# Kernel optimization log

Measured on AMD Instinct MI355X. Metric: run time of the kernel, lower is better.

The kernel has to match this reference:

```python
import jax, jax.numpy as jnp
import numpy as np

B, S, D, H = 2, 2048, 1024, 16
HD = D // H

def setup_inputs() -> dict:
    key = jax.random.key(0)
    ks = jax.random.split(key, 9)
    s = 1.0 / np.sqrt(D)
    inp = {"x": jax.random.normal(ks[0], (B, S, D), dtype=jnp.float32)}
    for i, name in enumerate(["q", "k", "v", "o"]):
        inp[f"W_{name}"] = jax.random.uniform(ks[1 + 2 * i], (D, D), dtype=jnp.float32, minval=-s, maxval=s)
        inp[f"b_{name}"] = jax.random.uniform(ks[2 + 2 * i], (D,), dtype=jnp.float32, minval=-s, maxval=s)
    return inp


def reference(x, W_q, b_q, W_k, b_k, W_v, b_v, W_o, b_o):
    # x: [B, S, D]
    def split_heads(t):
        return t.reshape(B, S, H, HD).transpose(0, 2, 1, 3)  # [B, H, S, HD]

    Q = split_heads(x @ W_q + b_q)
    K = split_heads(x @ W_k + b_k)
    V = split_heads(x @ W_v + b_v)

    scale = 1.0 / np.sqrt(HD).astype(np.float32)
    scores = jnp.einsum("bhqd,bhkd->bhqk", Q, K) * scale  # [B, H, S, S]
    weights = jax.nn.softmax(scores, axis=-1)
    attn = jnp.einsum("bhqk,bhkd->bhqd", weights, V)  # [B, H, S, HD]
    attn = attn.transpose(0, 2, 1, 3).reshape(B, S, D)
    return attn @ W_o + b_o
```

## Files before the change

kernel.cpp:

```cpp
#include <hip/hip_runtime.h>
#include <hip/hip_bf16.h>

#define BB 2
#define SS 2048
#define DD 1024
#define HH 16
#define HD 64

typedef __attribute__((ext_vector_type(8))) short bf16x8;
typedef __attribute__((ext_vector_type(4))) float f32x4;

__device__ __forceinline__ unsigned short f2bf(float f) {
  unsigned int u = __float_as_uint(f);
  return (unsigned short)((u + 0x7FFFu + ((u >> 16) & 1u)) >> 16);
}

__device__ __forceinline__ float fast_exp2(float x) {
#if __has_builtin(__builtin_amdgcn_exp2f)
  return __builtin_amdgcn_exp2f(x);
#else
  return __expf(x * 0.6931471805599453f);
#endif
}

__device__ __forceinline__ void async_copy16(const unsigned short* gp, unsigned short* lp) {
  __builtin_amdgcn_global_load_lds(
      (const __attribute__((address_space(1))) unsigned int*)gp,
      (__attribute__((address_space(3))) unsigned int*)lp, 16, 0, 0);
}

__device__ __forceinline__ void pl32_swap(unsigned& a, unsigned& b) {
#if __has_builtin(__builtin_amdgcn_permlane32_swap)
  auto r = __builtin_amdgcn_permlane32_swap(a, b, false, false);
  a = r[0];
  b = r[1];
#else
  asm volatile("v_permlane32_swap_b32 %0, %1" : "+v"(a), "+v"(b));
#endif
}
__device__ __forceinline__ void pl16_swap(unsigned& a, unsigned& b) {
#if __has_builtin(__builtin_amdgcn_permlane16_swap)
  auto r = __builtin_amdgcn_permlane16_swap(a, b, false, false);
  a = r[0];
  b = r[1];
#else
  asm volatile("v_permlane16_swap_b32 %0, %1" : "+v"(a), "+v"(b));
#endif
}

__global__ __launch_bounds__(256) void prep_kernel(
    const float* __restrict__ x, unsigned short* __restrict__ xb,
    const float* __restrict__ W0, unsigned short* __restrict__ T0,
    const float* __restrict__ W1, unsigned short* __restrict__ T1,
    const float* __restrict__ W2, unsigned short* __restrict__ T2,
    const float* __restrict__ W3, unsigned short* __restrict__ T3) {
  const int blk = blockIdx.x;
  const int t = threadIdx.x;
  if (blk < 4096) {
    int i = blk * 1024 + t * 4;
    float4 v = *(const float4*)(x + i);
    ushort4 u;
    u.x = f2bf(v.x); u.y = f2bf(v.y); u.z = f2bf(v.z); u.w = f2bf(v.w);
    *(ushort4*)(xb + i) = u;
    return;
  }
  const int j = blk - 4096;
  const int jw = j >> 10;
  const int tb = j & 1023;
  const float* W = jw == 0 ? W0 : (jw == 1 ? W1 : (jw == 2 ? W2 : W3));
  unsigned short* T = jw == 0 ? T0 : (jw == 1 ? T1 : (jw == 2 ? T2 : T3));
  __shared__ float tile[32][33];
  int k0 = (tb & 31) * 32, n0 = (tb >> 5) * 32;
  int c = t & 31, r0 = t >> 5;
#pragma unroll
  for (int i = 0; i < 4; ++i) {
    int r = r0 + i * 8;
    tile[r][c] = W[(size_t)(k0 + r) * DD + n0 + c];
  }
  __syncthreads();
#pragma unroll
  for (int i = 0; i < 4; ++i) {
    int r = r0 + i * 8;
    T[(size_t)(n0 + r) * DD + k0 + c] = f2bf(tile[c][r]);
  }
}

template <int STORE>
__device__ __forceinline__ void gemm_core(
    const unsigned short* __restrict__ A, const unsigned short* __restrict__ BT,
    const float* __restrict__ bias, void* __restrict__ outp, float scale,
    int bm, int bn) {
  const int t = threadIdx.x;
  const int w = t >> 6;
  const int l = t & 63;
  const int wm = (w >> 1) * 64;
  const int wn = (w & 1) * 64;

  __shared__ __align__(16) unsigned short As[128 * 32];
  __shared__ __align__(16) unsigned short Bs[128 * 32];

  f32x4 acc[4][4];
#pragma unroll
  for (int i = 0; i < 4; ++i)
#pragma unroll
    for (int j = 0; j < 4; ++j) acc[i][j] = (f32x4)0.f;

  const int fr = l & 15;
  const int kg = (l >> 4) * 8;

  for (int k0 = 0; k0 < DD; k0 += 32) {
    __syncthreads();
#pragma unroll
    for (int c = 0; c < 2; ++c) {
      int e = (w * 2 + c) * 512 + l * 8;
      int row = e >> 5, kk = e & 31;
      async_copy16(A + (size_t)(bm + row) * DD + k0 + kk, As + (w * 2 + c) * 512);
      async_copy16(BT + (size_t)(bn + row) * DD + k0 + kk, Bs + (w * 2 + c) * 512);
    }
    __syncthreads();

    bf16x8 af[4], bfr[4];
#pragma unroll
    for (int i = 0; i < 4; ++i)
      af[i] = *(const bf16x8*)(As + (wm + i * 16 + fr) * 32 + kg);
#pragma unroll
    for (int j = 0; j < 4; ++j)
      bfr[j] = *(const bf16x8*)(Bs + (wn + j * 16 + fr) * 32 + kg);
#pragma unroll
    for (int i = 0; i < 4; ++i)
#pragma unroll
      for (int j = 0; j < 4; ++j)
        acc[i][j] = __builtin_amdgcn_mfma_f32_16x16x32_bf16(af[i], bfr[j], acc[i][j], 0, 0, 0);
  }

  const int col_l = l & 15;
  const int row_l = (l >> 4) * 4;

#pragma unroll
  for (int i = 0; i < 4; ++i) {
    int m_base = bm + wm + i * 16 + row_l;
#pragma unroll
    for (int j = 0; j < 4; ++j) {
      int n = bn + wn + j * 16 + col_l;
      float bv = bias[n];
      float* out = (float*)outp;
#pragma unroll
      for (int r = 0; r < 4; ++r)
        out[(size_t)(m_base + r) * DD + n] = acc[i][j][r] + bv;
    }
  }
}

__global__ __launch_bounds__(256) void out_gemm_mfma(
    const unsigned short* __restrict__ A, const unsigned short* __restrict__ WoT,
    const float* __restrict__ bo, float* __restrict__ out) {
  const int i = blockIdx.x;
  const int xcd = i & 7;
  const int slot = i >> 3;
  const int bm = (xcd + 8 * (slot >> 3)) * 128;
  const int bn = (slot & 7) * 128;
  gemm_core<0>(A, WoT, bo, (void*)out, 1.0f, bm, bn);
}

__global__ __launch_bounds__(256, 3) void qkv_gemm_tri(
    const unsigned short* __restrict__ A,
    const unsigned short* __restrict__ WqT, const unsigned short* __restrict__ WkT,
    const unsigned short* __restrict__ WvT,
    const float* __restrict__ bq, const float* __restrict__ bk,
    const float* __restrict__ bv,
    unsigned short* __restrict__ Qo, unsigned short* __restrict__ Ko,
    unsigned short* __restrict__ VTo) {
  const int i = blockIdx.x;
  const int xcd = i & 7;
  const int slot = i >> 3;
  const int bm = (xcd + 8 * (slot / 24)) * 128;
  const int c = slot % 24;
  const int which = c >> 3;
  const int bn = (c & 7) * 128;
  const unsigned short* BT = which == 0 ? WqT : (which == 1 ? WkT : WvT);
  const float* bias = which == 0 ? bq : (which == 1 ? bk : bv);

  const int t = threadIdx.x;
  const int w = t >> 6;
  const int l = t & 63;
  const int wm = (w >> 1) * 64;
  const int wn = (w & 1) * 64;
  const int fr = l & 15;
  const int kgB = (l >> 4) * 16;

  __shared__ __align__(16) unsigned short lds[2][3][4096];

  f32x4 acc[4][4];
#pragma unroll
  for (int ii = 0; ii < 4; ++ii)
#pragma unroll
    for (int j = 0; j < 4; ++j) acc[ii][j] = (f32x4)0.f;

  int aoff[4], boff[4];
#pragma unroll
  for (int ii = 0; ii < 4; ++ii) {
    aoff[ii] = (wm + ii * 16 + fr) * 64 + kgB;
    boff[ii] = (wn + ii * 16 + fr) * 64 + kgB;
  }

  const int cc0 = w * 128 + l;
  const int cc1 = cc0 + 64;
  const int row0 = cc0 >> 2, kk0 = (cc0 & 3) * 8;
  const int row1 = cc1 >> 2, kk1 = (cc1 & 3) * 8;
  const unsigned short* a0 = A + (size_t)(bm + row0) * DD + kk0;
  const unsigned short* a1 = A + (size_t)(bm + row1) * DD + kk1;
  const unsigned short* b0 = BT + (size_t)(bn + row0) * DD + kk0;
  const unsigned short* b1 = BT + (size_t)(bn + row1) * DD + kk1;

  auto stage_tile = [&](int T) {
    if (T >= 32) return;
    const int buf = T % 3;
    const int k0 = T * 32;
    async_copy16(a0 + k0, &lds[0][buf][w * 1024]);
    async_copy16(a1 + k0, &lds[0][buf][w * 1024 + 512]);
    async_copy16(b0 + k0, &lds[1][buf][w * 1024]);
    async_copy16(b1 + k0, &lds[1][buf][w * 1024 + 512]);
  };

  auto phase = [&](int T, int vm) {
    const int buf = T % 3;
    const char* Ab = (const char*)&lds[0][buf][0];
    const char* Bb = (const char*)&lds[1][buf][0];
    bf16x8 af[4], bfr[4];
#pragma unroll
    for (int ii = 0; ii < 4; ++ii) af[ii] = *(const bf16x8*)(Ab + aoff[ii]);
#pragma unroll
    for (int j = 0; j < 4; ++j) bfr[j] = *(const bf16x8*)(Bb + boff[j]);
    stage_tile(T + 2);
    asm volatile("s_barrier" ::: "memory");
    __builtin_amdgcn_s_setprio(1);
#pragma unroll
    for (int ii = 0; ii < 4; ++ii)
#pragma unroll
      for (int j = 0; j < 4; ++j)
        acc[ii][j] = __builtin_amdgcn_mfma_f32_16x16x32_bf16(af[ii], bfr[j], acc[ii][j], 0, 0, 0);
    __builtin_amdgcn_s_setprio(0);
    if (vm == 1) asm volatile("s_waitcnt vmcnt(4)" ::: "memory");
    if (vm == 2) asm volatile("s_waitcnt vmcnt(0)" ::: "memory");
    asm volatile("s_barrier" ::: "memory");
  };

  stage_tile(0);
  stage_tile(1);
  asm volatile("s_waitcnt vmcnt(4)" ::: "memory");
  asm volatile("s_barrier" ::: "memory");

  for (int T = 0; T < 30; ++T) phase(T, 1);
  phase(30, 2);
  phase(31, 0);

  const int col_l = l & 15;
  const int row_l = (l >> 4) * 4;
  const int b_ = bm >> 11;

  if (which != 2) {
    const float scl = which == 0 ? 0.18033688011112042f : 1.0f;
    unsigned short* out = which == 0 ? Qo : Ko;
#pragma unroll
    for (int ii = 0; ii < 4; ++ii) {
      int m_base = bm + wm + ii * 16 + row_l;
#pragma unroll
      for (int j = 0; j < 4; ++j) {
        int n = bn + wn + j * 16 + col_l;
        float bv = bias[n];
        int h_ = n >> 6, hd_ = n & 63;
#pragma unroll
        for (int r = 0; r < 4; ++r) {
          int m = m_base + r;
          int b2 = m >> 11, s_ = m & 2047;
          out[(((size_t)(b2 * HH + h_) * SS) + s_) * HD + hd_] =
              f2bf((acc[ii][j][r] + bv) * scl);
        }
      }
    }
  } else {
    unsigned short* out = VTo;
    unsigned int* Tt = (unsigned int*)&lds[0][0][0];
    const int srow0 = bm & 2047;
#pragma unroll
    for (int p = 0; p < 4; ++p) {
      __syncthreads();
      if ((w & 1) == (p >> 1)) {
        const int jt0 = (p & 1) * 2;
#pragma unroll
        for (int jj = 0; jj < 2; ++jj) {
          int jt = jt0 + jj;
          int n_p = jj * 16 + col_l;
          float bv = bias[bn + p * 32 + n_p];
#pragma unroll
          for (int ii = 0; ii < 4; ++ii) {
            int m0 = wm + ii * 16 + row_l;
#pragma unroll
            for (int pr = 0; pr < 2; ++pr) {
              unsigned int val =
                  (unsigned int)f2bf(acc[ii][jt][2 * pr] + bv) |
                  ((unsigned int)f2bf(acc[ii][jt][2 * pr + 1] + bv) << 16);
              int m = m0 + 2 * pr;
              Tt[n_p * 64 + (((m >> 1)) ^ ((n_p & 7) << 2))] = val;
            }
          }
        }
      }
      __syncthreads();
#pragma unroll
      for (int cq = 0; cq < 2; ++cq) {
        int q = t + cq * 256;
        int n_p = q >> 4, cpos = q & 15;
        uint4 v = *(const uint4*)(Tt + n_p * 64 + ((cpos * 4) ^ ((n_p & 7) << 2)));
        int n_glob = bn + p * 32 + n_p;
        int h_ = n_glob >> 6, hd_ = n_glob & 63;
        *(uint4*)(out + ((size_t)((b_ * HH + h_) * HD + hd_)) * SS + srow0 + cpos * 8) = v;
      }
    }
  }
}

__global__ __launch_bounds__(512, 2) void flash_attn_mfma(
    const unsigned short* __restrict__ Q,
    const unsigned short* __restrict__ K,
    const unsigned short* __restrict__ VT,
    unsigned short* __restrict__ ctx) {
  const int bh = blockIdx.x;
  const int qt = blockIdx.y;
  const int b  = bh >> 4;
  const int h  = bh & 15;
  const int t  = threadIdx.x;
  const int w  = t >> 6;
  const int l  = t & 63;
  const int wg = w & 3;
  const int wh = w >> 2;
  const int g  = l >> 4;
  const int ln = l & 15;

  const unsigned short* Qp = Q + ((size_t)bh * SS + (size_t)qt * 128 + wg * 32) * HD;
  const unsigned short* Kp = K + (size_t)bh * SS * HD;
  const unsigned short* Vp = VT + (size_t)bh * HD * SS;

  __shared__ __align__(16) unsigned short smem[2][2][2][2048];
  __shared__ __align__(16) float rred[4 * 64 * 2];

  bf16x8 qf[2][2];
#pragma unroll
  for (int nt = 0; nt < 2; ++nt)
#pragma unroll
    for (int kb = 0; kb < 2; ++kb)
      qf[nt][kb] = *(const bf16x8*)(Qp + (nt * 16 + ln) * HD + kb * 32 + g * 8);

  f32x4 o[2][4];
#pragma unroll
  for (int nt = 0; nt < 2; ++nt)
#pragma unroll
    for (int mt = 0; mt < 4; ++mt) o[nt][mt] = (f32x4)0.f;
  float rs[2] = {0.f, 0.f};

  const int sp  = w >> 2;
  const int sq  = w & 3;
  const int idx = sq * 64 + l;
  const int rowK = idx >> 3;
  const int gccK = (idx & 7) ^ (rowK & 7);
  const unsigned short* kgp = Kp + (size_t)(sp * 32 + rowK) * HD + gccK * 8;
  const int rowV = idx >> 2;
  const int gc2V = (idx & 3) ^ ((rowV >> 1) & 3);
  const unsigned short* vgp = Vp + (size_t)rowV * SS + sp * 32 + gc2V * 8;
  unsigned short* dK = &smem[0][sp][0][sq * 512];
  unsigned short* dV = &smem[1][sp][0][sq * 512];

  int ko[2][2];
#pragma unroll
  for (int kb = 0; kb < 2; ++kb)
#pragma unroll
    for (int mt = 0; mt < 2; ++mt) {
      int row = mt * 16 + ln;
      ko[kb][mt] = row * 128 + (((kb * 4 + g) ^ (row & 7)) * 16);
    }
  int vo[4];
#pragma unroll
  for (int mt = 0; mt < 4; ++mt) {
    int row = mt * 16 + ln;
    vo[mt] = row * 64 + ((g ^ ((row >> 1) & 3)) * 16);
  }
  const char* kpar = (const char*)&smem[0][wh][0][0];
  const char* vpar = (const char*)&smem[1][wh][0][0];

  auto stage_i = [&](int db) {
    async_copy16(kgp, dK + db * 2048);
    async_copy16(vgp, dV + db * 2048);
    kgp += 64 * HD;
    vgp += 64;
  };

  auto body = [&](int db) {
    const char* Kst = kpar + db * 4096;
    const char* Vst = vpar + db * 4096;

    f32x4 st[2][2];
#pragma unroll
    for (int nt = 0; nt < 2; ++nt)
#pragma unroll
      for (int mt = 0; mt < 2; ++mt) st[nt][mt] = (f32x4)0.f;
#pragma unroll
    for (int kb = 0; kb < 2; ++kb)
#pragma unroll
      for (int mt = 0; mt < 2; ++mt) {
        bf16x8 ka = *(const bf16x8*)(Kst + ko[kb][mt]);
        st[0][mt] = __builtin_amdgcn_mfma_f32_16x16x32_bf16(ka, qf[0][kb], st[0][mt], 0, 0, 0);
        st[1][mt] = __builtin_amdgcn_mfma_f32_16x16x32_bf16(ka, qf[1][kb], st[1][mt], 0, 0, 0);
      }

    unsigned Sd[2][2][2];
#pragma unroll
    for (int nt = 0; nt < 2; ++nt) {
#pragma unroll
      for (int mt = 0; mt < 2; ++mt) {
        float p0 = fast_exp2(st[nt][mt][0]);
        float p1 = fast_exp2(st[nt][mt][1]);
        float p2 = fast_exp2(st[nt][mt][2]);
        float p3 = fast_exp2(st[nt][mt][3]);
        Sd[nt][mt][0] = __builtin_amdgcn_perm(__float_as_uint(p1), __float_as_uint(p0),
                                              0x07060302u);
        Sd[nt][mt][1] = __builtin_amdgcn_perm(__float_as_uint(p3), __float_as_uint(p2),
                                              0x07060302u);
        rs[nt] += (p0 + p1) + (p2 + p3);
      }
#pragma unroll
      for (int p = 0; p < 2; ++p) pl32_swap(Sd[nt][0][p], Sd[nt][1][p]);
#pragma unroll
      for (int p = 0; p < 2; ++p) pl16_swap(Sd[nt][0][p], Sd[nt][1][p]);
    }

    bf16x8 pbv[2];
#pragma unroll
    for (int nt = 0; nt < 2; ++nt) {
      union { unsigned u[4]; bf16x8 v; } cu;
      cu.u[0] = Sd[nt][0][0];
      cu.u[1] = Sd[nt][0][1];
      cu.u[2] = Sd[nt][1][0];
      cu.u[3] = Sd[nt][1][1];
      pbv[nt] = cu.v;
    }
#pragma unroll
    for (int mt = 0; mt < 4; ++mt) {
      bf16x8 va = *(const bf16x8*)(Vst + vo[mt]);
      o[0][mt] = __builtin_amdgcn_mfma_f32_16x16x32_bf16(va, pbv[0], o[0][mt], 0, 0, 0);
      o[1][mt] = __builtin_amdgcn_mfma_f32_16x16x32_bf16(va, pbv[1], o[1][mt], 0, 0, 0);
    }
  };

  stage_i(0);
  for (int kt2 = 0; kt2 < 16; ++kt2) {
    __syncthreads();
    stage_i(1);
    body(0);
    __syncthreads();
    if (kt2 < 15) stage_i(0);
    body(1);
  }

  __syncthreads();
  {
    float* ored = (float*)&smem[0][0][0][0];
    float* rb = ored + (wg * 64 + l) * 32;
    float* sb = rred + (wg * 64 + l) * 2;
    if (wh == 1) {
#pragma unroll
      for (int nt = 0; nt < 2; ++nt)
#pragma unroll
        for (int mt = 0; mt < 4; ++mt) {
          int idx2 = nt * 4 + mt;
          *(f32x4*)(rb + ((unsigned)(idx2 ^ (l & 7)) * 4)) = o[nt][mt];
        }
      sb[0] = rs[0];
      sb[1] = rs[1];
    }
    __syncthreads();
    if (wh == 1) return;
#pragma unroll
    for (int nt = 0; nt < 2; ++nt)
#pragma unroll
      for (int mt = 0; mt < 4; ++mt) {
        int idx2 = nt * 4 + mt;
        f32x4 pv = *(const f32x4*)(rb + ((unsigned)(idx2 ^ (l & 7)) * 4));
        o[nt][mt] += pv;
      }
    rs[0] += sb[0];
    rs[1] += sb[1];
  }

#pragma unroll
  for (int nt = 0; nt < 2; ++nt) {
    float lsum = rs[nt];
    lsum += __shfl_xor(lsum, 16, 64);
    lsum += __shfl_xor(lsum, 32, 64);
    float inv = 1.f / lsum;
    int srow = qt * 128 + wg * 32 + nt * 16 + ln;
    unsigned short* cb = ctx + (size_t)(b * SS + srow) * DD + h * HD;
#pragma unroll
    for (int mt = 0; mt < 4; ++mt) {
      ushort4 u4;
      u4.x = f2bf(o[nt][mt][0] * inv);
      u4.y = f2bf(o[nt][mt][1] * inv);
      u4.z = f2bf(o[nt][mt][2] * inv);
      u4.w = f2bf(o[nt][mt][3] * inv);
      *(ushort4*)(cb + mt * 16 + 4 * g) = u4;
    }
  }
}

extern "C" void kernel_launch(void* const* d_in, const int* in_sizes, int n_in,
                              void* d_out, int out_size, void* d_ws, size_t ws_size,
                              hipStream_t stream) {
  const float* x  = (const float*)d_in[0];
  const float* Wq = (const float*)d_in[1];
  const float* bq = (const float*)d_in[2];
  const float* Wk = (const float*)d_in[3];
  const float* bk = (const float*)d_in[4];
  const float* Wv = (const float*)d_in[5];
  const float* bv = (const float*)d_in[6];
  const float* Wo = (const float*)d_in[7];
  const float* bo = (const float*)d_in[8];
  float* out = (float*)d_out;

  const size_t ELEMS = (size_t)BB * SS * DD;
  char* ws = (char*)d_ws;
  unsigned short* xb   = (unsigned short*)ws;  ws += ELEMS * 2;
  unsigned short* WqT  = (unsigned short*)ws;  ws += (size_t)DD * DD * 2;
  unsigned short* WkT  = (unsigned short*)ws;  ws += (size_t)DD * DD * 2;
  unsigned short* WvT  = (unsigned short*)ws;  ws += (size_t)DD * DD * 2;
  unsigned short* WoT  = (unsigned short*)ws;  ws += (size_t)DD * DD * 2;
  unsigned short* Qb   = (unsigned short*)ws;  ws += ELEMS * 2;
  unsigned short* Kb   = (unsigned short*)ws;  ws += ELEMS * 2;
  unsigned short* VbT  = (unsigned short*)ws;  ws += ELEMS * 2;
  unsigned short* ctxb = (unsigned short*)ws;  ws += ELEMS * 2;

  prep_kernel<<<8192, 256, 0, stream>>>(x, xb, Wq, WqT, Wk, WkT, Wv, WvT, Wo, WoT);

  qkv_gemm_tri<<<768, 256, 0, stream>>>(xb, WqT, WkT, WvT, bq, bk, bv,
                                        Qb, Kb, VbT);

  dim3 attn_grid(BB * HH, SS / 128);
  flash_attn_mfma<<<attn_grid, 512, 0, stream>>>(Qb, Kb, VbT, ctxb);

  out_gemm_mfma<<<256, 256, 0, stream>>>(ctxb, WoT, bo, out);
}
```

Baseline: 185.4 us.

## Triple-buffer K/V staging with manual barriers, early LDS loads and setprio

Replaces the double-buffered K/V LDS pipeline with a three-stage ring. Each phase first loads all K and V fragments from LDS into registers, then issues the next async global copy, and runs the MFMA work at raised wave priority. Synchronisation moves from __syncthreads to raw s_barrier with explicit vmcnt waits, so global loads can stay in flight longer. This costs 50% more shared memory, which may lower occupancy, plus higher register pressure, and the hand-written wait counts must stay correct.

```diff
diff --git a/kernel.cpp b/kernel.cpp
--- a/kernel.cpp
+++ b/kernel.cpp
@@ -341,7 +341,7 @@
   const unsigned short* Kp = K + (size_t)bh * SS * HD;
   const unsigned short* Vp = VT + (size_t)bh * HD * SS;
 
-  __shared__ __align__(16) unsigned short smem[2][2][2][2048];
+  __shared__ __align__(16) unsigned short smem[2][2][3][2048];
   __shared__ __align__(16) float rred[4 * 64 * 2];
 
   bf16x8 qf[2][2];
@@ -387,16 +387,29 @@
   const char* kpar = (const char*)&smem[0][wh][0][0];
   const char* vpar = (const char*)&smem[1][wh][0][0];
 
-  auto stage_i = [&](int db) {
-    async_copy16(kgp, dK + db * 2048);
-    async_copy16(vgp, dV + db * 2048);
+  auto stage_i = [&](int buf) {
+    async_copy16(kgp, dK + buf * 2048);
+    async_copy16(vgp, dV + buf * 2048);
     kgp += 64 * HD;
     vgp += 64;
   };
 
-  auto body = [&](int db) {
-    const char* Kst = kpar + db * 4096;
-    const char* Vst = vpar + db * 4096;
+  auto phase = [&](int buf, int sbuf, bool doStage, int vm) {
+    const char* Kst = kpar + buf * 4096;
+    const char* Vst = vpar + buf * 4096;
+
+    bf16x8 ka[2][2], va[4];
+#pragma unroll
+    for (int kb = 0; kb < 2; ++kb)
+#pragma unroll
+      for (int mt = 0; mt < 2; ++mt)
+        ka[kb][mt] = *(const bf16x8*)(Kst + ko[kb][mt]);
+#pragma unroll
+    for (int mt = 0; mt < 4; ++mt) va[mt] = *(const bf16x8*)(Vst + vo[mt]);
+
+    if (doStage) stage_i(sbuf);
+    asm volatile("s_barrier" ::: "memory");
+    __builtin_amdgcn_s_setprio(1);
 
     f32x4 st[2][2];
 #pragma unroll
@@ -407,9 +420,8 @@
     for (int kb = 0; kb < 2; ++kb)
 #pragma unroll
       for (int mt = 0; mt < 2; ++mt) {
-        bf16x8 ka = *(const bf16x8*)(Kst + ko[kb][mt]);
-        st[0][mt] = __builtin_amdgcn_mfma_f32_16x16x32_bf16(ka, qf[0][kb], st[0][mt], 0, 0, 0);
-        st[1][mt] = __builtin_amdgcn_mfma_f32_16x16x32_bf16(ka, qf[1][kb], st[1][mt], 0, 0, 0);
+        st[0][mt] = __builtin_amdgcn_mfma_f32_16x16x32_bf16(ka[kb][mt], qf[0][kb], st[0][mt], 0, 0, 0);
+        st[1][mt] = __builtin_amdgcn_mfma_f32_16x16x32_bf16(ka[kb][mt], qf[1][kb], st[1][mt], 0, 0, 0);
       }
 
     unsigned Sd[2][2][2];
@@ -445,21 +457,28 @@
     }
 #pragma unroll
     for (int mt = 0; mt < 4; ++mt) {
-      bf16x8 va = *(const bf16x8*)(Vst + vo[mt]);
-      o[0][mt] = __builtin_amdgcn_mfma_f32_16x16x32_bf16(va, pbv[0], o[0][mt], 0, 0, 0);
-      o[1][mt] = __builtin_amdgcn_mfma_f32_16x16x32_bf16(va, pbv[1], o[1][mt], 0, 0, 0);
-    }
+      o[0][mt] = __builtin_amdgcn_mfma_f32_16x16x32_bf16(va[mt], pbv[0], o[0][mt], 0, 0, 0);
+      o[1][mt] = __builtin_amdgcn_mfma_f32_16x16x32_bf16(va[mt], pbv[1], o[1][mt], 0, 0, 0);
+    }
+
+    __builtin_amdgcn_s_setprio(0);
+    if (vm == 1) asm volatile("s_waitcnt vmcnt(2)" ::: "memory");
+    if (vm == 2) asm volatile("s_waitcnt vmcnt(0)" ::: "memory");
+    asm volatile("s_barrier" ::: "memory");
   };
 
   stage_i(0);
-  for (int kt2 = 0; kt2 < 16; ++kt2) {
-    __syncthreads();
-    stage_i(1);
-    body(0);
-    __syncthreads();
-    if (kt2 < 15) stage_i(0);
-    body(1);
-  }
+  stage_i(1);
+  asm volatile("s_waitcnt vmcnt(2)" ::: "memory");
+  asm volatile("s_barrier" ::: "memory");
+
+  for (int it = 0; it < 10; ++it) {
+    phase(0, 2, true, 1);
+    phase(1, 0, true, 1);
+    phase(2, 1, true, 1);
+  }
+  phase(0, 0, false, 2);
+  phase(1, 0, false, 0);
 
   __syncthreads();
   {
```

After: 185.5 us. No clear change (+0.0%).
